# Kernel tuning notes

Hardware: AMD Instinct MI355X
Metric: run time of the kernel (lower is better)

## Reference

```python
import jax, jax.numpy as jnp
import numpy as np

B, T, H = 32, 2048, 512
D = 2 * H  # bidirectional encoder feature dim


def setup_inputs() -> dict:
    key = jax.random.key(0)
    k1, k2, k3, k4, k5 = jax.random.split(key, 5)
    stdv = 1.0 / np.sqrt(H)
    return {
        "hidden": jax.random.normal(k1, (B, D), dtype=jnp.float32),
        "encoder_outputs": jax.random.normal(k2, (B, T, D), dtype=jnp.float32),
        "W_attn": jax.random.normal(k3, (H, 2 * D), dtype=jnp.float32) * stdv,
        "b_attn": jax.random.normal(k4, (H,), dtype=jnp.float32) * stdv,
        "v": jax.random.normal(k5, (H,), dtype=jnp.float32) * stdv,
    }


def reference(hidden, encoder_outputs, W_attn, b_attn, v):
    # The original per-timestep sliding-window loop recomputes a position-wise
    # Linear+tanh+dot whose value is independent of the window index, and
    # overlapping writes overwrite with identical values. The exact same math
    # is full additive attention over all T positions.
    d = encoder_outputs.shape[-1]
    Wh = W_attn[:, :d]   # acts on repeated decoder hidden state
    We = W_attn[:, d:]   # acts on encoder outputs
    # [B, H] ; avoids materializing the [B, T, 4H] concat
    hid_proj = jnp.einsum('bd,hd->bh', hidden, Wh)
    # [B, T, H]
    energy = jnp.tanh(jnp.einsum('btd,hd->bth', encoder_outputs, We)
                      + hid_proj[:, None, :] + b_attn)
    scores = jnp.einsum('bth,h->bt', energy, v)  # [B, T]
    return jax.nn.softmax(scores, axis=1)[:, None, :]  # [B, 1, T]
```

## Files before the change

kernel.cpp:

```cpp
#include <hip/hip_runtime.h>

#define Bv 32
#define Tv 2048
#define Hv 512
#define Dv 1024

using bf16x8 = __attribute__((ext_vector_type(8))) __bf16;
using bf16x4 = __attribute__((ext_vector_type(4))) __bf16;
using f32x4  = __attribute__((ext_vector_type(4))) float;

__global__ void swizzle_we(const float* __restrict__ W, bf16x8* __restrict__ We_sw) {
    int g = blockIdx.x * 256 + threadIdx.x;
    int h = g >> 7;
    int d = (g & 127) * 8;
    const float* src = W + h * (2 * Dv) + Dv + d;
    float4 f0 = *(const float4*)src;
    float4 f1 = *(const float4*)(src + 4);
    bf16x8 o;
    o[0] = (__bf16)f0.x; o[1] = (__bf16)f0.y; o[2] = (__bf16)f0.z; o[3] = (__bf16)f0.w;
    o[4] = (__bf16)f1.x; o[5] = (__bf16)f1.y; o[6] = (__bf16)f1.z; o[7] = (__bf16)f1.w;
    int s = ((h >> 4) * 32 + (d >> 5)) * 64 + (((d >> 3) & 3) << 4) + (h & 15);
    We_sw[s] = o;
}

__global__ void hid_proj_kernel(const float* __restrict__ hidden,
                                const float* __restrict__ W,
                                const float* __restrict__ b_attn,
                                float* __restrict__ hp) {
    int h   = blockIdx.x;
    int tid = threadIdx.x;
    float4 wh = ((const float4*)(W + h * (2 * Dv)))[tid];
    __shared__ float red[4][Bv];
    int lane = tid & 63, w = tid >> 6;
    for (int b = 0; b < Bv; ++b) {
        float4 x = ((const float4*)(hidden + b * Dv))[tid];
        float p = wh.x * x.x + wh.y * x.y + wh.z * x.z + wh.w * x.w;
#pragma unroll
        for (int m = 1; m < 64; m <<= 1) p += __shfl_xor(p, m);
        if (lane == 0) red[w][b] = p;
    }
    __syncthreads();
    if (tid < Bv)
        hp[tid * Hv + h] = red[0][tid] + red[1][tid] + red[2][tid] + red[3][tid] + b_attn[h];
}

__device__ __forceinline__ float fast_tanh(float x) {
    float xc = fminf(fmaxf(x, -9.0f), 9.0f);
    float e  = __expf(2.0f * xc);
    return 1.0f - 2.0f / (e + 1.0f);
}

__global__ __launch_bounds__(512) void attn_main(
    const float* __restrict__ enc, const bf16x8* __restrict__ Bg,
    const float* __restrict__ hp, const float* __restrict__ vvec,
    float* __restrict__ scores)
{
    __shared__ __align__(16) __bf16 Abuf[2][64 * 72];
    __shared__ float redbuf[8][64];

    const int tid   = threadIdx.x;
    const int lane  = tid & 63;
    const int w     = tid >> 6;
    const int row0  = blockIdx.x * 64;
    const int batch = row0 >> 11;

    const int srow = tid >> 3;
    const int sd0  = (tid & 7) * 4;
    const float* gA = enc + (row0 + srow) * Dv + sd0;
    __bf16* lw0 = &Abuf[0][srow * 72 + sd0];

    const bf16x8* Bptr = Bg + (w * 4 * 32) * 64 + lane;

    f32x4 acc[4][4];
#pragma unroll
    for (int i = 0; i < 4; ++i)
#pragma unroll
        for (int j = 0; j < 4; ++j)
            acc[i][j] = (f32x4){0.f, 0.f, 0.f, 0.f};

    float4 f0 = *(const float4*)gA;
    float4 f1 = *(const float4*)(gA + 32);
    bf16x8 Bc[2][4];
#pragma unroll
    for (int ktl = 0; ktl < 2; ++ktl)
#pragma unroll
        for (int j = 0; j < 4; ++j)
            Bc[ktl][j] = Bptr[(j * 32 + ktl) * 64];

    const int arow  = lane & 15;
    const int acol8 = (lane >> 4) * 8;

    for (int kc = 0; kc < 16; ++kc) {
        __bf16* p = lw0 + (kc & 1) * (64 * 72);
        bf16x4 o0, o1;
        o0[0] = (__bf16)f0.x; o0[1] = (__bf16)f0.y; o0[2] = (__bf16)f0.z; o0[3] = (__bf16)f0.w;
        o1[0] = (__bf16)f1.x; o1[1] = (__bf16)f1.y; o1[2] = (__bf16)f1.z; o1[3] = (__bf16)f1.w;
        *(bf16x4*)p        = o0;
        *(bf16x4*)(p + 32) = o1;
        if (kc < 15) {
            f0 = *(const float4*)(gA + (kc + 1) * 64);
            f1 = *(const float4*)(gA + (kc + 1) * 64 + 32);
        }
        __syncthreads();

        bf16x8 Bn[2][4];
        if (kc < 15) {
#pragma unroll
            for (int ktl = 0; ktl < 2; ++ktl)
#pragma unroll
                for (int j = 0; j < 4; ++j)
                    Bn[ktl][j] = Bptr[(j * 32 + (kc + 1) * 2 + ktl) * 64];
        }

        const __bf16* rb = &Abuf[kc & 1][0];
#pragma unroll
        for (int ktl = 0; ktl < 2; ++ktl) {
            bf16x8 a0 = *(const bf16x8*)(rb + (0 * 16 + arow) * 72 + ktl * 32 + acol8);
            bf16x8 a1 = *(const bf16x8*)(rb + (1 * 16 + arow) * 72 + ktl * 32 + acol8);
            bf16x8 a2 = *(const bf16x8*)(rb + (2 * 16 + arow) * 72 + ktl * 32 + acol8);
            bf16x8 a3 = *(const bf16x8*)(rb + (3 * 16 + arow) * 72 + ktl * 32 + acol8);
#pragma unroll
            for (int j = 0; j < 4; ++j) {
                acc[0][j] = __builtin_amdgcn_mfma_f32_16x16x32_bf16(a0, Bc[ktl][j], acc[0][j], 0, 0, 0);
                acc[1][j] = __builtin_amdgcn_mfma_f32_16x16x32_bf16(a1, Bc[ktl][j], acc[1][j], 0, 0, 0);
                acc[2][j] = __builtin_amdgcn_mfma_f32_16x16x32_bf16(a2, Bc[ktl][j], acc[2][j], 0, 0, 0);
                acc[3][j] = __builtin_amdgcn_mfma_f32_16x16x32_bf16(a3, Bc[ktl][j], acc[3][j], 0, 0, 0);
            }
        }
#pragma unroll
        for (int ktl = 0; ktl < 2; ++ktl)
#pragma unroll
            for (int j = 0; j < 4; ++j)
                Bc[ktl][j] = Bn[ktl][j];
    }

    float hpv[4], vv[4];
#pragma unroll
    for (int j = 0; j < 4; ++j) {
        int n  = w * 64 + j * 16 + (lane & 15);
        hpv[j] = hp[batch * Hv + n];
        vv[j]  = vvec[n];
    }
    const int qrow = (lane >> 4) * 4;
#pragma unroll
    for (int mt = 0; mt < 4; ++mt)
#pragma unroll
        for (int r = 0; r < 4; ++r) {
            float p = 0.f;
#pragma unroll
            for (int j = 0; j < 4; ++j)
                p += vv[j] * fast_tanh(acc[mt][j][r] + hpv[j]);
            p += __shfl_xor(p, 1);
            p += __shfl_xor(p, 2);
            p += __shfl_xor(p, 4);
            p += __shfl_xor(p, 8);
            if ((lane & 15) == 0)
                redbuf[w][mt * 16 + qrow + r] = p;
        }
    __syncthreads();
    if (tid < 64) {
        float s = 0.f;
#pragma unroll
        for (int ww = 0; ww < 8; ++ww) s += redbuf[ww][tid];
        scores[row0 + tid] = s;
    }
}

__global__ void softmax_kernel(const float* __restrict__ scores, float* __restrict__ out) {
    int b   = blockIdx.x;
    int tid = threadIdx.x;
    const float* s = scores + b * Tv;
    float local[8];
    float m = -1e30f;
#pragma unroll
    for (int i = 0; i < 8; ++i) { local[i] = s[tid + i * 256]; m = fmaxf(m, local[i]); }
    __shared__ float red[4];
    int lane = tid & 63, w = tid >> 6;
#pragma unroll
    for (int x = 1; x < 64; x <<= 1) m = fmaxf(m, __shfl_xor(m, x));
    if (lane == 0) red[w] = m;
    __syncthreads();
    m = fmaxf(fmaxf(red[0], red[1]), fmaxf(red[2], red[3]));
    float sum = 0.f;
#pragma unroll
    for (int i = 0; i < 8; ++i) { local[i] = expf(local[i] - m); sum += local[i]; }
#pragma unroll
    for (int x = 1; x < 64; x <<= 1) sum += __shfl_xor(sum, x);
    __syncthreads();
    if (lane == 0) red[w] = sum;
    __syncthreads();
    sum = red[0] + red[1] + red[2] + red[3];
    float inv = 1.0f / sum;
#pragma unroll
    for (int i = 0; i < 8; ++i) out[b * Tv + tid + i * 256] = local[i] * inv;
}

extern "C" void kernel_launch(void* const* d_in, const int* in_sizes, int n_in,
                              void* d_out, int out_size, void* d_ws, size_t ws_size,
                              hipStream_t stream) {
    const float* hidden = (const float*)d_in[0];
    const float* enc    = (const float*)d_in[1];
    const float* W      = (const float*)d_in[2];
    const float* b_attn = (const float*)d_in[3];
    const float* v      = (const float*)d_in[4];
    float* out = (float*)d_out;

    char* ws = (char*)d_ws;
    bf16x8* We_sw = (bf16x8*)ws;
    float*  hp    = (float*)(ws + (1 << 20));
    float*  sc    = (float*)(ws + (1 << 20) + (1 << 16));

    swizzle_we<<<256, 256, 0, stream>>>(W, We_sw);
    hid_proj_kernel<<<Hv, 256, 0, stream>>>(hidden, W, b_attn, hp);
    attn_main<<<(Bv * Tv) / 64, 512, 0, stream>>>(enc, We_sw, hp, v, sc);
    softmax_kernel<<<Bv, 256, 0, stream>>>(sc, out);
}
```

Before: 444.3 us.

## Fuse prep kernels, process four row tiles per block with wider K chunks

Merges the weight swizzle and hidden projection into one prep kernel, removing a launch. The main kernel now handles 256 rows per block as four sequential 64-row tiles. Each K chunk is widened to 128, halving the barrier count per tile, and the next tile's first A chunk is prefetched. Softmax moves to 512 threads with __expf. The risk is fewer blocks (256) on a GPU with many CUs, which may lower occupancy and latency hiding in this memory-bound kernel.

```diff
diff --git a/kernel.cpp b/kernel.cpp
--- a/kernel.cpp
+++ b/kernel.cpp
@@ -9,26 +9,26 @@
 using bf16x4 = __attribute__((ext_vector_type(4))) __bf16;
 using f32x4  = __attribute__((ext_vector_type(4))) float;
 
-__global__ void swizzle_we(const float* __restrict__ W, bf16x8* __restrict__ We_sw) {
-    int g = blockIdx.x * 256 + threadIdx.x;
-    int h = g >> 7;
-    int d = (g & 127) * 8;
-    const float* src = W + h * (2 * Dv) + Dv + d;
-    float4 f0 = *(const float4*)src;
-    float4 f1 = *(const float4*)(src + 4);
-    bf16x8 o;
-    o[0] = (__bf16)f0.x; o[1] = (__bf16)f0.y; o[2] = (__bf16)f0.z; o[3] = (__bf16)f0.w;
-    o[4] = (__bf16)f1.x; o[5] = (__bf16)f1.y; o[6] = (__bf16)f1.z; o[7] = (__bf16)f1.w;
-    int s = ((h >> 4) * 32 + (d >> 5)) * 64 + (((d >> 3) & 3) << 4) + (h & 15);
-    We_sw[s] = o;
-}
-
-__global__ void hid_proj_kernel(const float* __restrict__ hidden,
-                                const float* __restrict__ W,
-                                const float* __restrict__ b_attn,
-                                float* __restrict__ hp) {
+__global__ void prep_kernel(const float* __restrict__ hidden,
+                            const float* __restrict__ W,
+                            const float* __restrict__ b_attn,
+                            bf16x8* __restrict__ We_sw,
+                            float* __restrict__ hp) {
     int h   = blockIdx.x;
     int tid = threadIdx.x;
+
+    if (tid < 128) {
+        int d = tid * 8;
+        const float* src = W + h * (2 * Dv) + Dv + d;
+        float4 f0 = *(const float4*)src;
+        float4 f1 = *(const float4*)(src + 4);
+        bf16x8 o;
+        o[0] = (__bf16)f0.x; o[1] = (__bf16)f0.y; o[2] = (__bf16)f0.z; o[3] = (__bf16)f0.w;
+        o[4] = (__bf16)f1.x; o[5] = (__bf16)f1.y; o[6] = (__bf16)f1.z; o[7] = (__bf16)f1.w;
+        int s = ((h >> 4) * 32 + (d >> 5)) * 64 + (((d >> 3) & 3) << 4) + (h & 15);
+        We_sw[s] = o;
+    }
+
     float4 wh = ((const float4*)(W + h * (2 * Dv)))[tid];
     __shared__ float red[4][Bv];
     int lane = tid & 63, w = tid >> 6;
@@ -55,31 +55,30 @@
     const float* __restrict__ hp, const float* __restrict__ vvec,
     float* __restrict__ scores)
 {
-    __shared__ __align__(16) __bf16 Abuf[2][64 * 72];
+    __shared__ __align__(16) __bf16 Abuf[2][64 * 136];
     __shared__ float redbuf[8][64];
 
-    const int tid   = threadIdx.x;
-    const int lane  = tid & 63;
-    const int w     = tid >> 6;
-    const int row0  = blockIdx.x * 64;
-    const int batch = row0 >> 11;
+    const int tid  = threadIdx.x;
+    const int lane = tid & 63;
+    const int w    = tid >> 6;
 
     const int srow = tid >> 3;
     const int sd0  = (tid & 7) * 4;
-    const float* gA = enc + (row0 + srow) * Dv + sd0;
-    __bf16* lw0 = &Abuf[0][srow * 72 + sd0];
+    __bf16* lw0 = &Abuf[0][srow * 136 + sd0];
 
     const bf16x8* Bptr = Bg + (w * 4 * 32) * 64 + lane;
 
-    f32x4 acc[4][4];
-#pragma unroll
-    for (int i = 0; i < 4; ++i)
-#pragma unroll
-        for (int j = 0; j < 4; ++j)
-            acc[i][j] = (f32x4){0.f, 0.f, 0.f, 0.f};
-
-    float4 f0 = *(const float4*)gA;
-    float4 f1 = *(const float4*)(gA + 32);
+    const int arow  = lane & 15;
+    const int acol8 = (lane >> 4) * 8;
+
+    const int row0 = blockIdx.x * 256;
+
+    float4 f[4];
+    {
+        const float* gA = enc + (row0 + srow) * Dv + sd0;
+#pragma unroll
+        for (int s = 0; s < 4; ++s) f[s] = *(const float4*)(gA + s * 32);
+    }
     bf16x8 Bc[2][4];
 #pragma unroll
     for (int ktl = 0; ktl < 2; ++ktl)
@@ -87,82 +86,114 @@
         for (int j = 0; j < 4; ++j)
             Bc[ktl][j] = Bptr[(j * 32 + ktl) * 64];
 
-    const int arow  = lane & 15;
-    const int acol8 = (lane >> 4) * 8;
-
-    for (int kc = 0; kc < 16; ++kc) {
-        __bf16* p = lw0 + (kc & 1) * (64 * 72);
-        bf16x4 o0, o1;
-        o0[0] = (__bf16)f0.x; o0[1] = (__bf16)f0.y; o0[2] = (__bf16)f0.z; o0[3] = (__bf16)f0.w;
-        o1[0] = (__bf16)f1.x; o1[1] = (__bf16)f1.y; o1[2] = (__bf16)f1.z; o1[3] = (__bf16)f1.w;
-        *(bf16x4*)p        = o0;
-        *(bf16x4*)(p + 32) = o1;
-        if (kc < 15) {
-            f0 = *(const float4*)(gA + (kc + 1) * 64);
-            f1 = *(const float4*)(gA + (kc + 1) * 64 + 32);
-        }
+    for (int tile = 0; tile < 4; ++tile) {
+        const int trow0  = row0 + tile * 64;
+        const int batch  = trow0 >> 11;
+        const float* gAt = enc + (trow0 + srow) * Dv + sd0;
+
+        f32x4 acc[4][4];
+#pragma unroll
+        for (int i = 0; i < 4; ++i)
+#pragma unroll
+            for (int j = 0; j < 4; ++j)
+                acc[i][j] = (f32x4){0.f, 0.f, 0.f, 0.f};
+
+        for (int kc = 0; kc < 8; ++kc) {
+            __bf16* p = lw0 + (kc & 1) * (64 * 136);
+#pragma unroll
+            for (int s = 0; s < 4; ++s) {
+                bf16x4 o;
+                o[0] = (__bf16)f[s].x; o[1] = (__bf16)f[s].y;
+                o[2] = (__bf16)f[s].z; o[3] = (__bf16)f[s].w;
+                *(bf16x4*)(p + s * 32) = o;
+            }
+            if (kc < 7) {
+#pragma unroll
+                for (int s = 0; s < 4; ++s)
+                    f[s] = *(const float4*)(gAt + (kc + 1) * 128 + s * 32);
+            } else if (tile < 3) {
+                const float* gAn = enc + (trow0 + 64 + srow) * Dv + sd0;
+#pragma unroll
+                for (int s = 0; s < 4; ++s)
+                    f[s] = *(const float4*)(gAn + s * 32);
+            }
+            __syncthreads();
+
+            const __bf16* rb = &Abuf[kc & 1][0];
+#pragma unroll
+            for (int hk = 0; hk < 2; ++hk) {
+                bf16x8 Bn[2][4];
+                const int ktn = kc * 4 + (hk + 1) * 2;
+                if (ktn < 32) {
+#pragma unroll
+                    for (int ktl = 0; ktl < 2; ++ktl)
+#pragma unroll
+                        for (int j = 0; j < 4; ++j)
+                            Bn[ktl][j] = Bptr[(j * 32 + ktn + ktl) * 64];
+                }
+#pragma unroll
+                for (int ktl = 0; ktl < 2; ++ktl) {
+                    const int kofs = (hk * 2 + ktl) * 32;
+                    bf16x8 a0 = *(const bf16x8*)(rb + (0 * 16 + arow) * 136 + kofs + acol8);
+                    bf16x8 a1 = *(const bf16x8*)(rb + (1 * 16 + arow) * 136 + kofs + acol8);
+                    bf16x8 a2 = *(const bf16x8*)(rb + (2 * 16 + arow) * 136 + kofs + acol8);
+                    bf16x8 a3 = *(const bf16x8*)(rb + (3 * 16 + arow) * 136 + kofs + acol8);
+#pragma unroll
+                    for (int j = 0; j < 4; ++j) {
+                        acc[0][j] = __builtin_amdgcn_mfma_f32_16x16x32_bf16(a0, Bc[ktl][j], acc[0][j], 0, 0, 0);
+                        acc[1][j] = __builtin_amdgcn_mfma_f32_16x16x32_bf16(a1, Bc[ktl][j], acc[1][j], 0, 0, 0);
+                        acc[2][j] = __builtin_amdgcn_mfma_f32_16x16x32_bf16(a2, Bc[ktl][j], acc[2][j], 0, 0, 0);
+                        acc[3][j] = __builtin_amdgcn_mfma_f32_16x16x32_bf16(a3, Bc[ktl][j], acc[3][j], 0, 0, 0);
+                    }
+                }
+                if (ktn < 32) {
+#pragma unroll
+                    for (int ktl = 0; ktl < 2; ++ktl)
+#pragma unroll
+                        for (int j = 0; j < 4; ++j)
+                            Bc[ktl][j] = Bn[ktl][j];
+                }
+            }
+        }
+
+        if (tile < 3) {
+#pragma unroll
+            for (int ktl = 0; ktl < 2; ++ktl)
+#pragma unroll
+                for (int j = 0; j < 4; ++j)
+                    Bc[ktl][j] = Bptr[(j * 32 + ktl) * 64];
+        }
+
+        float hpv[4], vv[4];
+#pragma unroll
+        for (int j = 0; j < 4; ++j) {
+            int n  = w * 64 + j * 16 + (lane & 15);
+            hpv[j] = hp[batch * Hv + n];
+            vv[j]  = vvec[n];
+        }
+        const int qrow = (lane >> 4) * 4;
+#pragma unroll
+        for (int mt = 0; mt < 4; ++mt)
+#pragma unroll
+            for (int r = 0; r < 4; ++r) {
+                float p = 0.f;
+#pragma unroll
+                for (int j = 0; j < 4; ++j)
+                    p += vv[j] * fast_tanh(acc[mt][j][r] + hpv[j]);
+                p += __shfl_xor(p, 1);
+                p += __shfl_xor(p, 2);
+                p += __shfl_xor(p, 4);
+                p += __shfl_xor(p, 8);
+                if ((lane & 15) == 0)
+                    redbuf[w][mt * 16 + qrow + r] = p;
+            }
         __syncthreads();
-
-        bf16x8 Bn[2][4];
-        if (kc < 15) {
-#pragma unroll
-            for (int ktl = 0; ktl < 2; ++ktl)
-#pragma unroll
-                for (int j = 0; j < 4; ++j)
-                    Bn[ktl][j] = Bptr[(j * 32 + (kc + 1) * 2 + ktl) * 64];
-        }
-
-        const __bf16* rb = &Abuf[kc & 1][0];
-#pragma unroll
-        for (int ktl = 0; ktl < 2; ++ktl) {
-            bf16x8 a0 = *(const bf16x8*)(rb + (0 * 16 + arow) * 72 + ktl * 32 + acol8);
-            bf16x8 a1 = *(const bf16x8*)(rb + (1 * 16 + arow) * 72 + ktl * 32 + acol8);
-            bf16x8 a2 = *(const bf16x8*)(rb + (2 * 16 + arow) * 72 + ktl * 32 + acol8);
-            bf16x8 a3 = *(const bf16x8*)(rb + (3 * 16 + arow) * 72 + ktl * 32 + acol8);
-#pragma unroll
-            for (int j = 0; j < 4; ++j) {
-                acc[0][j] = __builtin_amdgcn_mfma_f32_16x16x32_bf16(a0, Bc[ktl][j], acc[0][j], 0, 0, 0);
-                acc[1][j] = __builtin_amdgcn_mfma_f32_16x16x32_bf16(a1, Bc[ktl][j], acc[1][j], 0, 0, 0);
-                acc[2][j] = __builtin_amdgcn_mfma_f32_16x16x32_bf16(a2, Bc[ktl][j], acc[2][j], 0, 0, 0);
-                acc[3][j] = __builtin_amdgcn_mfma_f32_16x16x32_bf16(a3, Bc[ktl][j], acc[3][j], 0, 0, 0);
-            }
-        }
-#pragma unroll
-        for (int ktl = 0; ktl < 2; ++ktl)
-#pragma unroll
-            for (int j = 0; j < 4; ++j)
-                Bc[ktl][j] = Bn[ktl][j];
-    }
-
-    float hpv[4], vv[4];
-#pragma unroll
-    for (int j = 0; j < 4; ++j) {
-        int n  = w * 64 + j * 16 + (lane & 15);
-        hpv[j] = hp[batch * Hv + n];
-        vv[j]  = vvec[n];
-    }
-    const int qrow = (lane >> 4) * 4;
-#pragma unroll
-    for (int mt = 0; mt < 4; ++mt)
-#pragma unroll
-        for (int r = 0; r < 4; ++r) {
-            float p = 0.f;
-#pragma unroll
-            for (int j = 0; j < 4; ++j)
-                p += vv[j] * fast_tanh(acc[mt][j][r] + hpv[j]);
-            p += __shfl_xor(p, 1);
-            p += __shfl_xor(p, 2);
-            p += __shfl_xor(p, 4);
-            p += __shfl_xor(p, 8);
-            if ((lane & 15) == 0)
-                redbuf[w][mt * 16 + qrow + r] = p;
-        }
-    __syncthreads();
-    if (tid < 64) {
-        float s = 0.f;
-#pragma unroll
-        for (int ww = 0; ww < 8; ++ww) s += redbuf[ww][tid];
-        scores[row0 + tid] = s;
+        if (tid < 64) {
+            float s = 0.f;
+#pragma unroll
+            for (int ww = 0; ww < 8; ++ww) s += redbuf[ww][tid];
+            scores[trow0 + tid] = s;
+        }
     }
 }
 
@@ -170,29 +201,32 @@
     int b   = blockIdx.x;
     int tid = threadIdx.x;
     const float* s = scores + b * Tv;
-    float local[8];
+    float local[4];
     float m = -1e30f;
 #pragma unroll
-    for (int i = 0; i < 8; ++i) { local[i] = s[tid + i * 256]; m = fmaxf(m, local[i]); }
-    __shared__ float red[4];
+    for (int i = 0; i < 4; ++i) { local[i] = s[tid + i * 512]; m = fmaxf(m, local[i]); }
+    __shared__ float red[8];
     int lane = tid & 63, w = tid >> 6;
 #pragma unroll
     for (int x = 1; x < 64; x <<= 1) m = fmaxf(m, __shfl_xor(m, x));
     if (lane == 0) red[w] = m;
     __syncthreads();
-    m = fmaxf(fmaxf(red[0], red[1]), fmaxf(red[2], red[3]));
+#pragma unroll
+    for (int ww = 0; ww < 8; ++ww) m = fmaxf(m, red[ww]);
     float sum = 0.f;
 #pragma unroll
-    for (int i = 0; i < 8; ++i) { local[i] = expf(local[i] - m); sum += local[i]; }
+    for (int i = 0; i < 4; ++i) { local[i] = __expf(local[i] - m); sum += local[i]; }
 #pragma unroll
     for (int x = 1; x < 64; x <<= 1) sum += __shfl_xor(sum, x);
     __syncthreads();
     if (lane == 0) red[w] = sum;
     __syncthreads();
-    sum = red[0] + red[1] + red[2] + red[3];
+    sum = 0.f;
+#pragma unroll
+    for (int ww = 0; ww < 8; ++ww) sum += red[ww];
     float inv = 1.0f / sum;
 #pragma unroll
-    for (int i = 0; i < 8; ++i) out[b * Tv + tid + i * 256] = local[i] * inv;
+    for (int i = 0; i < 4; ++i) out[b * Tv + tid + i * 512] = local[i] * inv;
 }
 
 extern "C" void kernel_launch(void* const* d_in, const int* in_sizes, int n_in,
@@ -210,8 +244,7 @@
     float*  hp    = (float*)(ws + (1 << 20));
     float*  sc    = (float*)(ws + (1 << 20) + (1 << 16));
 
-    swizzle_we<<<256, 256, 0, stream>>>(W, We_sw);
-    hid_proj_kernel<<<Hv, 256, 0, stream>>>(hidden, W, b_attn, hp);
-    attn_main<<<(Bv * Tv) / 64, 512, 0, stream>>>(enc, We_sw, hp, v, sc);
-    softmax_kernel<<<Bv, 256, 0, stream>>>(sc, out);
-}
+    prep_kernel<<<Hv, 256, 0, stream>>>(hidden, W, b_attn, We_sw, hp);
+    attn_main<<<(Bv * Tv) / 256, 512, 0, stream>>>(enc, We_sw, hp, v, sc);
+    softmax_kernel<<<Bv, 512, 0, stream>>>(sc, out);
+}
```

Result: slower. 643.3 us (+44.8%).
